# Optimization experiments

Measured on AMD Instinct MI355X. Metric: run time of the kernel, lower is better.

## Reference

```python
import jax, jax.numpy as jnp
import numpy as np

N = 8192      # nodes
E = 262144    # edges per graph (avg degree 32)
D_IN = 256
HID = 64
HEADS = 2
NEG_SLOPE = 0.2  # PyG GATConv leaky_relu slope


def _self_loops(ei, n):
    loop = jnp.arange(n, dtype=ei.dtype)
    return jnp.concatenate([ei[0], loop]), jnp.concatenate([ei[1], loop])


def gat_conv(x, src, dst, W, att_src, att_dst, b, concat):
    # PyG GATConv: h=[N,H,C]; alpha=softmax_dst(leaky_relu(a_s[src]+a_d[dst]))
    n = x.shape[0]
    H, C = att_src.shape
    h = (x @ W).reshape(n, H, C)
    a_s = (h * att_src).sum(-1)           # [N,H]
    a_d = (h * att_dst).sum(-1)           # [N,H]
    e = jax.nn.leaky_relu(a_s[src] + a_d[dst], NEG_SLOPE)  # [Etot,H]
    e = e - jax.ops.segment_max(e, dst, num_segments=n)[dst]
    e = jnp.exp(e)
    denom = jax.ops.segment_sum(e, dst, num_segments=n)[dst] + 1e-16
    alpha = e / denom                     # edge softmax per target node
    msg = h[src] * alpha[:, :, None]      # [Etot,H,C]
    out = jax.ops.segment_sum(msg, dst, num_segments=n)  # [N,H,C]
    out = out.reshape(n, H * C) if concat else out.mean(axis=1)
    return out + b


def gcn_conv(x, src, dst, W, b):
    # PyG GCNConv: D^{-1/2}(A+I)D^{-1/2} X W + b (self loops already appended)
    n = x.shape[0]
    h = x @ W
    deg = jax.ops.segment_sum(jnp.ones_like(src, jnp.float32), dst, num_segments=n)
    dinv = jax.lax.rsqrt(jnp.maximum(deg, 1.0))
    norm = dinv[src] * dinv[dst]          # [Etot]
    return jax.ops.segment_sum(h[src] * norm[:, None], dst, num_segments=n) + b


def cross_attn(q_in, kv_in, Wq, bq, Wk, bk, Wv, bv, Wo, bo, num_heads):
    n, d = q_in.shape
    hd = d // num_heads
    q = (q_in @ Wq + bq).reshape(n, num_heads, hd)
    k = (kv_in @ Wk + bk).reshape(n, num_heads, hd)
    v = (kv_in @ Wv + bv).reshape(n, num_heads, hd)
    scores = jnp.einsum('qhd,khd->hqk', q, k) / np.sqrt(hd).astype(np.float32)
    attn = jax.nn.softmax(scores, axis=-1)                 # [H,N,N]
    out = jnp.einsum('hqk,khd->qhd', attn, v).reshape(n, d) @ Wo + bo
    weights = attn.mean(axis=0)[None]                      # [1,N,N] avg heads (torch default)
    return out, weights


def setup_inputs():
    key = jax.random.key(0)
    ks = jax.random.split(key, 24)
    w = lambda k, s: jax.random.normal(k, s, jnp.float32) * 0.05
    inp = {
        'x': jax.random.normal(ks[0], (N, D_IN), jnp.float32),
        'edge_index_tkg': jax.random.randint(ks[1], (2, E), 0, N, jnp.int64 if jax.config.jax_enable_x64 else jnp.int32),
        'edge_index_ekg': jax.random.randint(ks[2], (2, E), 0, N, jnp.int64 if jax.config.jax_enable_x64 else jnp.int32),
        # GAT layer 1: heads=2, concat=True
        'gat1_W': w(ks[3], (D_IN, HEADS * HID)),
        'gat1_att_src': w(ks[4], (HEADS, HID)),
        'gat1_att_dst': w(ks[5], (HEADS, HID)),
        'gat1_b': jnp.zeros((HEADS * HID,), jnp.float32),
        # GAT layer 2: heads=1, concat=False
        'gat2_W': w(ks[6], (HEADS * HID, HID)),
        'gat2_att_src': w(ks[7], (1, HID)),
        'gat2_att_dst': w(ks[8], (1, HID)),
        'gat2_b': jnp.zeros((HID,), jnp.float32),
        # GCN layers
        'gcn1_W': w(ks[9], (D_IN, HID)),
        'gcn1_b': jnp.zeros((HID,), jnp.float32),
        'gcn2_W': w(ks[10], (HID, HID)),
        'gcn2_b': jnp.zeros((HID,), jnp.float32),
        # cross attention (hidden=64, 2 heads)
        'Wq': w(ks[11], (HID, HID)), 'bq': jnp.zeros((HID,), jnp.float32),
        'Wk': w(ks[12], (HID, HID)), 'bk': jnp.zeros((HID,), jnp.float32),
        'Wv': w(ks[13], (HID, HID)), 'bv': jnp.zeros((HID,), jnp.float32),
        'Wo': w(ks[14], (HID, HID)), 'bo': jnp.zeros((HID,), jnp.float32),
        # MLP head
        'fc1_W': w(ks[15], (2 * HID, HID)), 'fc1_b': jnp.zeros((HID,), jnp.float32),
        'fc2_W': w(ks[16], (HID, 1)), 'fc2_b': jnp.zeros((1,), jnp.float32),
    }
    return inp


def reference(x, edge_index_tkg, edge_index_ekg,
              gat1_W, gat1_att_src, gat1_att_dst, gat1_b,
              gat2_W, gat2_att_src, gat2_att_dst, gat2_b,
              gcn1_W, gcn1_b, gcn2_W, gcn2_b,
              Wq, bq, Wk, bk, Wv, bv, Wo, bo,
              fc1_W, fc1_b, fc2_W, fc2_b):
    n = x.shape[0]
    src_t, dst_t = _self_loops(edge_index_tkg, n)
    src_e, dst_e = _self_loops(edge_index_ekg, n)

    h_tkg = jax.nn.elu(gat_conv(x, src_t, dst_t, gat1_W, gat1_att_src, gat1_att_dst, gat1_b, True))
    h_tkg = jax.nn.elu(gat_conv(h_tkg, src_t, dst_t, gat2_W, gat2_att_src, gat2_att_dst, gat2_b, False))

    h_ekg = jax.nn.relu(gcn_conv(x, src_e, dst_e, gcn1_W, gcn1_b))
    h_ekg = jax.nn.relu(gcn_conv(h_ekg, src_e, dst_e, gcn2_W, gcn2_b))

    h_attn, attn_weights = cross_attn(h_tkg, h_ekg, Wq, bq, Wk, bk, Wv, bv, Wo, bo, HEADS)

    h_fused = jnp.concatenate([h_tkg, h_attn], axis=1)   # [N, 2*HID]
    pred = (jax.nn.relu(h_fused @ fc1_W + fc1_b) @ fc2_W + fc2_b).squeeze(-1)
    return pred, attn_weights
```

## Files before the change

kernel.cpp:

```cpp
#include <hip/hip_runtime.h>
#include <cstdint>
#include <cstddef>

#define NN 8192
#define EE 262144
#define ET 270336

using short8  = __attribute__((ext_vector_type(8))) short;
using floatx4 = __attribute__((ext_vector_type(4))) float;

__device__ __forceinline__ unsigned short f2bf(float f) {
  unsigned int u = __float_as_uint(f);
  u += 0x7fffu + ((u >> 16) & 1u);
  return (unsigned short)(u >> 16);
}

__global__ void edge_hist2_k(const int* __restrict__ ei_t, const int* __restrict__ ei_e,
                             int* __restrict__ cnt_t, int* __restrict__ cnt_e) {
  int idx = blockIdx.x * 256 + threadIdx.x;
  int g = idx >= ET;
  int e = g ? idx - ET : idx;
  const int* ei = g ? ei_e : ei_t;
  int* cnt = g ? cnt_e : cnt_t;
  int d = (e < EE) ? ei[EE + e] : (e - EE);
  atomicAdd(&cnt[d], 1);
}

__global__ void scan2_k(int* cnt_t, int* off_t, int* cnt_e, int* off_e) {
  int* cnt = blockIdx.x ? cnt_e : cnt_t;
  int* off = blockIdx.x ? off_e : off_t;
  __shared__ int s[1024];
  int t = threadIdx.x;
  int v[8]; int base = t * 8; int sum = 0;
  #pragma unroll
  for (int j = 0; j < 8; ++j) { v[j] = cnt[base + j]; sum += v[j]; }
  s[t] = sum; __syncthreads();
  for (int o = 1; o < 1024; o <<= 1) {
    int x = (t >= o) ? s[t - o] : 0;
    __syncthreads();
    s[t] += x;
    __syncthreads();
  }
  int excl = s[t] - sum;
  #pragma unroll
  for (int j = 0; j < 8; ++j) { off[base + j] = excl; cnt[base + j] = excl; excl += v[j]; }
  if (t == 1023) off[NN] = excl;
}

__global__ void edge_scatter2_k(const int* __restrict__ ei_t, const int* __restrict__ ei_e,
                                int* __restrict__ pos_t, int* __restrict__ pos_e,
                                int* __restrict__ srcs_t, int* __restrict__ srcs_e) {
  int idx = blockIdx.x * 256 + threadIdx.x;
  int g = idx >= ET;
  int e = g ? idx - ET : idx;
  const int* ei = g ? ei_e : ei_t;
  int* pos = g ? pos_e : pos_t;
  int* srcs = g ? srcs_e : srcs_t;
  int sv, d;
  if (e < EE) { sv = ei[e]; d = ei[EE + e]; } else { sv = d = e - EE; }
  int p = atomicAdd(&pos[d], 1);
  srcs[p] = sv;
}

__device__ __forceinline__ void gemm_core(const float* __restrict__ A, int lda, int K,
                                          const float* __restrict__ Bs, int row0, int col,
                                          float acc[8]) {
  #pragma unroll
  for (int r = 0; r < 8; ++r) acc[r] = 0.f;
  for (int k = 0; k < K; k += 4) {
    float b0 = Bs[(k + 0) * 32 + col], b1 = Bs[(k + 1) * 32 + col];
    float b2 = Bs[(k + 2) * 32 + col], b3 = Bs[(k + 3) * 32 + col];
    #pragma unroll
    for (int r = 0; r < 8; ++r) {
      const float4 a4 = *(const float4*)(A + (size_t)(row0 + r) * lda + k);
      acc[r] = fmaf(a4.x, b0, acc[r]);
      acc[r] = fmaf(a4.y, b1, acc[r]);
      acc[r] = fmaf(a4.z, b2, acc[r]);
      acc[r] = fmaf(a4.w, b3, acc[r]);
    }
  }
}

__global__ __launch_bounds__(256) void mm_x_k(const float* __restrict__ x,
    const float* __restrict__ Wgat, const float* __restrict__ Wgcn,
    const float* __restrict__ as_w, const float* __restrict__ ad_w,
    float* __restrict__ h1, float* __restrict__ hg1,
    float* __restrict__ a_s1, float* __restrict__ a_d1) {
  __shared__ float Bs[256 * 32];
  const int tid = threadIdx.x, by = blockIdx.y;
  const bool gat = by < 4;
  const int NC = gat ? 128 : 64;
  const int c0 = gat ? by * 32 : (by - 4) * 32;
  const float* B = gat ? Wgat : Wgcn;
  for (int idx = tid; idx < 256 * 32; idx += 256)
    Bs[idx] = B[(idx >> 5) * NC + c0 + (idx & 31)];
  __syncthreads();
  const int row0 = blockIdx.x * 64 + (tid >> 5) * 8;
  const int col = tid & 31;
  float acc[8];
  gemm_core(x, 256, 256, Bs, row0, col, acc);
  if (gat) {
    #pragma unroll
    for (int r = 0; r < 8; ++r) h1[(size_t)(row0 + r) * 128 + c0 + col] = acc[r];
    const int head = c0 >> 6;
    const float asw = as_w[head * 64 + (c0 & 63) + col];
    const float adw = ad_w[head * 64 + (c0 & 63) + col];
    float ps[8], pd[8];
    #pragma unroll
    for (int r = 0; r < 8; ++r) { ps[r] = acc[r] * asw; pd[r] = acc[r] * adw; }
    #pragma unroll
    for (int m = 16; m >= 1; m >>= 1)
      #pragma unroll
      for (int r = 0; r < 8; ++r) { ps[r] += __shfl_xor(ps[r], m); pd[r] += __shfl_xor(pd[r], m); }
    if (col == 0) {
      #pragma unroll
      for (int r = 0; r < 8; ++r) {
        atomicAdd(&a_s1[(row0 + r) * 2 + head], ps[r]);
        atomicAdd(&a_d1[(row0 + r) * 2 + head], pd[r]);
      }
    }
  } else {
    #pragma unroll
    for (int r = 0; r < 8; ++r) hg1[(size_t)(row0 + r) * 64 + c0 + col] = acc[r];
  }
}

template<int H, int C>
__device__ __forceinline__ void gat_agg_body(const float* __restrict__ h,
    const float* __restrict__ a_s, const float* __restrict__ a_d,
    const int* __restrict__ off, const int* __restrict__ srcs,
    const float* __restrict__ bias, float* __restrict__ out, int ldout, int b) {
  constexpr int HC = H * C;
  const int tid = threadIdx.x;
  const int hd = tid / C;
  const int r0 = off[b], r1 = off[b + 1];
  __shared__ int s_src[HC];
  __shared__ float s_w[HC][H];
  float ad[H];
  #pragma unroll
  for (int hh = 0; hh < H; ++hh) ad[hh] = a_d[b * H + hh];
  float acc = 0.f, den = 0.f;
  for (int base = r0; base < r1; base += HC) {
    __syncthreads();
    int e = base + tid;
    if (e < r1) {
      int sv = srcs[e];
      s_src[tid] = sv;
      #pragma unroll
      for (int hh = 0; hh < H; ++hh) {
        float xv = a_s[sv * H + hh] + ad[hh];
        xv = xv > 0.f ? xv : 0.2f * xv;
        s_w[tid][hh] = __expf(xv);
      }
    }
    __syncthreads();
    int cnt = min(HC, r1 - base);
    for (int j = 0; j < cnt; ++j) {
      float wv = s_w[j][hd];
      den += wv;
      acc = fmaf(wv, h[(size_t)s_src[j] * HC + tid], acc);
    }
  }
  float o = acc / den + bias[tid];
  out[(size_t)b * ldout + tid] = o > 0.f ? o : (__expf(o) - 1.f);
}

template<int H, int C>
__global__ void gat_agg_k(const float* __restrict__ h, const float* __restrict__ a_s,
                          const float* __restrict__ a_d, const int* __restrict__ off,
                          const int* __restrict__ srcs, const float* __restrict__ bias,
                          float* __restrict__ out, int ldout) {
  gat_agg_body<H, C>(h, a_s, a_d, off, srcs, bias, out, ldout, blockIdx.x);
}

__global__ __launch_bounds__(128) void agg1_k(
    const float* __restrict__ h1, const float* __restrict__ a_s1, const float* __restrict__ a_d1,
    const int* __restrict__ off_t, const int* __restrict__ src_t,
    const float* __restrict__ gat1_b, float* __restrict__ g1out,
    const float* __restrict__ hg1, const int* __restrict__ off_e, const int* __restrict__ src_e,
    const float* __restrict__ gcn1_b, const float* __restrict__ gcn2_W, float* __restrict__ h2g) {
  const int tid = threadIdx.x;
  if (blockIdx.x < NN) {
    gat_agg_body<2, 64>(h1, a_s1, a_d1, off_t, src_t, gat1_b, g1out, 128, blockIdx.x);
  } else {
    const int nb = (blockIdx.x - NN) * 2;
    const int sub = tid >> 6, t = tid & 63;
    const int node = nb + sub;
    __shared__ int s_src2[2][64];
    __shared__ float s_nrm2[2][64];
    __shared__ float s_row2[2][64];
    const int r0 = off_e[node], r1 = off_e[node + 1];
    const int cA = off_e[nb + 1] - off_e[nb];
    const int cB = off_e[nb + 2] - off_e[nb + 1];
    const int trips = (max(cA, cB) + 63) >> 6;
    float dinv_b = rsqrtf((float)max(r1 - r0, 1));
    float acc = 0.f;
    for (int it = 0; it < trips; ++it) {
      __syncthreads();
      int e = r0 + it * 64 + t;
      if (e < r1) {
        int sv = src_e[e];
        s_src2[sub][t] = sv;
        int ds = off_e[sv + 1] - off_e[sv];
        s_nrm2[sub][t] = dinv_b * rsqrtf((float)max(ds, 1));
      }
      __syncthreads();
      int cnt = min(64, r1 - (r0 + it * 64));
      for (int j = 0; j < cnt; ++j)
        acc = fmaf(s_nrm2[sub][j], hg1[(size_t)s_src2[sub][j] * 64 + t], acc);
    }
    s_row2[sub][t] = fmaxf(acc + gcn1_b[t], 0.f);
    __syncthreads();
    float acc2 = 0.f;
    for (int k = 0; k < 64; ++k)
      acc2 = fmaf(s_row2[sub][k], gcn2_W[k * 64 + t], acc2);
    h2g[(size_t)node * 64 + t] = acc2;
  }
}

__global__ __launch_bounds__(256) void mm2_k(
    const float* __restrict__ g1out, const float* __restrict__ gat2_W,
    const float* __restrict__ gat2_as, const float* __restrict__ gat2_ad,
    float* __restrict__ h2, float* __restrict__ a_s2, float* __restrict__ a_d2,
    const float* __restrict__ h2g, const int* __restrict__ off_e, const int* __restrict__ src_e,
    const float* __restrict__ gcn2_b, float* __restrict__ hekg) {
  const int tid = threadIdx.x;
  if (blockIdx.x < 256) {
    __shared__ float Bs[128 * 32];
    const int bx = blockIdx.x & 127;
    const int c0 = (blockIdx.x >> 7) * 32;
    for (int idx = tid; idx < 128 * 32; idx += 256)
      Bs[idx] = gat2_W[(idx >> 5) * 64 + c0 + (idx & 31)];
    __syncthreads();
    const int row0 = bx * 64 + (tid >> 5) * 8;
    const int col = tid & 31;
    float acc[8];
    gemm_core(g1out, 128, 128, Bs, row0, col, acc);
    const float asw = gat2_as[c0 + col];
    const float adw = gat2_ad[c0 + col];
    float ps[8], pd[8];
    #pragma unroll
    for (int r = 0; r < 8; ++r) {
      h2[(size_t)(row0 + r) * 64 + c0 + col] = acc[r];
      ps[r] = acc[r] * asw; pd[r] = acc[r] * adw;
    }
    #pragma unroll
    for (int m = 16; m >= 1; m >>= 1)
      #pragma unroll
      for (int r = 0; r < 8; ++r) { ps[r] += __shfl_xor(ps[r], m); pd[r] += __shfl_xor(pd[r], m); }
    if (col == 0) {
      #pragma unroll
      for (int r = 0; r < 8; ++r) {
        atomicAdd(&a_s2[row0 + r], ps[r]);
        atomicAdd(&a_d2[row0 + r], pd[r]);
      }
    }
  } else {
    const int nb = (blockIdx.x - 256) * 4;
    const int sub = tid >> 6, t = tid & 63;
    const int node = nb + sub;
    __shared__ int s_src4[4][64];
    __shared__ float s_nrm4[4][64];
    const int r0 = off_e[node], r1 = off_e[node + 1];
    int cmax = 0;
    #pragma unroll
    for (int i = 0; i < 4; ++i) cmax = max(cmax, off_e[nb + i + 1] - off_e[nb + i]);
    const int trips = (cmax + 63) >> 6;
    float dinv_b = rsqrtf((float)max(r1 - r0, 1));
    float acc = 0.f;
    for (int it = 0; it < trips; ++it) {
      __syncthreads();
      int e = r0 + it * 64 + t;
      if (e < r1) {
        int sv = src_e[e];
        s_src4[sub][t] = sv;
        int ds = off_e[sv + 1] - off_e[sv];
        s_nrm4[sub][t] = dinv_b * rsqrtf((float)max(ds, 1));
      }
      __syncthreads();
      int cnt = min(64, r1 - (r0 + it * 64));
      for (int j = 0; j < cnt; ++j)
        acc = fmaf(s_nrm4[sub][j], h2g[(size_t)s_src4[sub][j] * 64 + t], acc);
    }
    hekg[(size_t)node * 64 + t] = fmaxf(acc + gcn2_b[t], 0.f);
  }
}

__global__ __launch_bounds__(256) void mm_qkv_k(const float* __restrict__ htkg,
    const float* __restrict__ hekg,
    const float* __restrict__ Wq, const float* __restrict__ bq,
    const float* __restrict__ Wk, const float* __restrict__ bk,
    const float* __restrict__ Wv, const float* __restrict__ bv,
    unsigned short* __restrict__ qb, unsigned short* __restrict__ kb,
    unsigned short* __restrict__ Vt) {
  __shared__ float Bs[64 * 32];
  __shared__ float Ts[32][65];
  const int tid = threadIdx.x, by = blockIdx.y;
  const int kind = by >> 1;
  const int c0 = (by & 1) * 32;
  const float* A = (kind == 0) ? htkg : hekg;
  const float* B = (kind == 0) ? Wq : (kind == 1) ? Wk : Wv;
  const float* bias = (kind == 0) ? bq : (kind == 1) ? bk : bv;
  for (int idx = tid; idx < 64 * 32; idx += 256)
    Bs[idx] = B[(idx >> 5) * 64 + c0 + (idx & 31)];
  __syncthreads();
  const int row0 = blockIdx.x * 64 + (tid >> 5) * 8;
  const int col = tid & 31;
  float acc[8];
  gemm_core(A, 64, 64, Bs, row0, col, acc);
  const float bb = bias[c0 + col];
  if (kind == 0) {
    const float SCL = 0.17677669529663687f * 1.4426950408889634f;
    #pragma unroll
    for (int r = 0; r < 8; ++r)
      qb[(size_t)(row0 + r) * 64 + c0 + col] = f2bf((acc[r] + bb) * SCL);
  } else if (kind == 1) {
    #pragma unroll
    for (int r = 0; r < 8; ++r)
      kb[(size_t)(row0 + r) * 64 + c0 + col] = f2bf(acc[r] + bb);
  } else {
    const int rl = (tid >> 5) * 8;
    #pragma unroll
    for (int r = 0; r < 8; ++r) Ts[col][rl + r] = acc[r] + bb;
    __syncthreads();
    const int c = tid >> 3, rr = (tid & 7) * 8;
    short8 pk;
    #pragma unroll
    for (int j = 0; j < 8; ++j) pk[j] = (short)f2bf(Ts[c][rr + j]);
    *(short8*)(Vt + (size_t)(c0 + c) * NN + blockIdx.x * 64 + rr) = pk;
  }
}

__global__ __launch_bounds__(256, 4) void att_pass1(const unsigned short* __restrict__ qb,
                                                    const unsigned short* __restrict__ kb,
                                                    float* __restrict__ lrow) {
  const int tid = threadIdx.x;
  const int lane = tid & 63, wv = tid >> 6;
  const int ql = lane & 15, quad = lane >> 4;
  const int qt0 = (blockIdx.x >> 1) * 16;
  const int khalf = blockIdx.x & 1;
  const floatx4 zf = {0.f, 0.f, 0.f, 0.f};
  short8 qf[2];
  #pragma unroll
  for (int h = 0; h < 2; ++h)
    qf[h] = *(const short8*)(qb + (size_t)(qt0 + ql) * 64 + h * 32 + quad * 8);
  float lacc[2][4];
  #pragma unroll
  for (int h = 0; h < 2; ++h)
    #pragma unroll
    for (int r = 0; r < 4; ++r) lacc[h][r] = 0.f;
  int kbase = khalf * 4096 + wv * 1024;
  for (int it = 0; it < 32; ++it, kbase += 32) {
    short8 kf[2][2];
    #pragma unroll
    for (int kt = 0; kt < 2; ++kt)
      #pragma unroll
      for (int h = 0; h < 2; ++h)
        kf[kt][h] = *(const short8*)(kb + (size_t)(kbase + kt * 16 + ql) * 64 + h * 32 + quad * 8);
    #pragma unroll
    for (int h = 0; h < 2; ++h)
      #pragma unroll
      for (int kt = 0; kt < 2; ++kt) {
        floatx4 s = __builtin_amdgcn_mfma_f32_16x16x32_bf16(qf[h], kf[kt][h], zf, 0, 0, 0);
        #pragma unroll
        for (int r = 0; r < 4; ++r) lacc[h][r] += __builtin_amdgcn_exp2f(s[r]);
      }
  }
  #pragma unroll
  for (int o = 8; o >= 1; o >>= 1)
    #pragma unroll
    for (int h = 0; h < 2; ++h)
      #pragma unroll
      for (int r = 0; r < 4; ++r)
        lacc[h][r] += __shfl_xor(lacc[h][r], o, 16);
  if (ql == 0) {
    #pragma unroll
    for (int h = 0; h < 2; ++h)
      #pragma unroll
      for (int r = 0; r < 4; ++r)
        atomicAdd(&lrow[(size_t)(qt0 + quad * 4 + r) * 2 + h], lacc[h][r]);
  }
}

__global__ __launch_bounds__(256, 4) void att_pass2(
    const unsigned short* __restrict__ qb, const unsigned short* __restrict__ kb,
    const unsigned short* __restrict__ Vt, const float* __restrict__ lrow,
    float* __restrict__ attn, float* __restrict__ Opart) {
  __shared__ __align__(16) float Esh[4][2][16 * 36];
  __shared__ float Osh[16 * 64];
  const int tid = threadIdx.x;
  const int lane = tid & 63, wv = tid >> 6;
  const int ql = lane & 15, quad = lane >> 4;
  const int qt0 = (blockIdx.x >> 1) * 16;
  const int khalf = blockIdx.x & 1;
  float* O = Opart + (size_t)khalf * NN * 64;
  const floatx4 zf = {0.f, 0.f, 0.f, 0.f};

  for (int idx = tid; idx < 16 * 64; idx += 256) Osh[idx] = 0.f;
  __syncthreads();

  short8 qf[2];
  #pragma unroll
  for (int h = 0; h < 2; ++h)
    qf[h] = *(const short8*)(qb + (size_t)(qt0 + ql) * 64 + h * 32 + quad * 8);

  float invl[2][4];
  #pragma unroll
  for (int h = 0; h < 2; ++h)
    #pragma unroll
    for (int r = 0; r < 4; ++r)
      invl[h][r] = 1.0f / lrow[(size_t)(qt0 + quad * 4 + r) * 2 + h];

  floatx4 oacc[2][2];
  #pragma unroll
  for (int h = 0; h < 2; ++h)
    #pragma unroll
    for (int hf = 0; hf < 2; ++hf) oacc[h][hf] = zf;

  int kbase = khalf * 4096 + wv * 1024;
  for (int it = 0; it < 32; ++it, kbase += 32) {
    short8 kf[2][2], vf[2][2];
    #pragma unroll
    for (int kt = 0; kt < 2; ++kt)
      #pragma unroll
      for (int h = 0; h < 2; ++h)
        kf[kt][h] = *(const short8*)(kb + (size_t)(kbase + kt * 16 + ql) * 64 + h * 32 + quad * 8);
    #pragma unroll
    for (int h = 0; h < 2; ++h)
      #pragma unroll
      for (int hf = 0; hf < 2; ++hf)
        vf[h][hf] = *(const short8*)(Vt + (size_t)(h * 32 + hf * 16 + ql) * NN + kbase + quad * 8);

    floatx4 p[2][2];
    #pragma unroll
    for (int h = 0; h < 2; ++h)
      #pragma unroll
      for (int kt = 0; kt < 2; ++kt) {
        floatx4 s = __builtin_amdgcn_mfma_f32_16x16x32_bf16(qf[h], kf[kt][h], zf, 0, 0, 0);
        #pragma unroll
        for (int r = 0; r < 4; ++r)
          p[h][kt][r] = __builtin_amdgcn_exp2f(s[r]) * invl[h][r];
      }
    #pragma unroll
    for (int kt = 0; kt < 2; ++kt)
      #pragma unroll
      for (int r = 0; r < 4; ++r) {
        size_t row = (size_t)(qt0 + quad * 4 + r);
        __builtin_nontemporal_store(0.5f * (p[0][kt][r] + p[1][kt][r]),
                                    &attn[row * NN + kbase + kt * 16 + ql]);
      }
    #pragma unroll
    for (int h = 0; h < 2; ++h)
      #pragma unroll
      for (int kt = 0; kt < 2; ++kt)
        #pragma unroll
        for (int r = 0; r < 4; ++r)
          Esh[wv][h][(quad * 4 + r) * 36 + kt * 16 + ql] = p[h][kt][r];
    #pragma unroll
    for (int h = 0; h < 2; ++h) {
      const float* ep = &Esh[wv][h][ql * 36 + quad * 8];
      float4 x0 = *(const float4*)ep;
      float4 x1 = *(const float4*)(ep + 4);
      short8 ef;
      ef[0] = (short)f2bf(x0.x); ef[1] = (short)f2bf(x0.y);
      ef[2] = (short)f2bf(x0.z); ef[3] = (short)f2bf(x0.w);
      ef[4] = (short)f2bf(x1.x); ef[5] = (short)f2bf(x1.y);
      ef[6] = (short)f2bf(x1.z); ef[7] = (short)f2bf(x1.w);
      #pragma unroll
      for (int hf = 0; hf < 2; ++hf)
        oacc[h][hf] = __builtin_amdgcn_mfma_f32_16x16x32_bf16(ef, vf[h][hf], oacc[h][hf], 0, 0, 0);
    }
  }
  #pragma unroll
  for (int h = 0; h < 2; ++h)
    #pragma unroll
    for (int hf = 0; hf < 2; ++hf)
      #pragma unroll
      for (int r = 0; r < 4; ++r)
        atomicAdd(&Osh[(quad * 4 + r) * 64 + h * 32 + hf * 16 + ql], oacc[h][hf][r]);
  __syncthreads();
  for (int idx = tid; idx < 16 * 64; idx += 256)
    O[(size_t)qt0 * 64 + idx] = Osh[idx];
}

__global__ __launch_bounds__(256) void tail_k(const float* __restrict__ Opart,
    const float* __restrict__ htkg, const float* __restrict__ Wo, const float* __restrict__ bo,
    const float* __restrict__ fc1W, const float* __restrict__ fc1b,
    const float* __restrict__ fc2W, const float* __restrict__ fc2b,
    float* __restrict__ pred) {
  __shared__ float Ws[8192];
  __shared__ float T1[2048];
  __shared__ float T2[2048];
  const int tid = threadIdx.x;
  const int col = tid & 63, rg = tid >> 6;
  const int rowbase = blockIdx.x * 32;
  for (int i = tid; i < 2048; i += 256) {
    size_t idx = (size_t)rowbase * 64 + i;
    T1[i] = Opart[idx] + Opart[(size_t)NN * 64 + idx];
  }
  for (int i = tid; i < 4096; i += 256) Ws[i] = Wo[i];
  const float rbo = bo[col], rf1b = fc1b[col], rf2 = fc2W[col], rf2b = fc2b[0];
  __syncthreads();
  float ha[8];
  #pragma unroll
  for (int r = 0; r < 8; ++r) {
    const int row = rg * 8 + r;
    float acc = rbo;
    for (int k = 0; k < 64; ++k) acc = fmaf(T1[row * 64 + k], Ws[k * 64 + col], acc);
    ha[r] = acc;
  }
  __syncthreads();
  #pragma unroll
  for (int r = 0; r < 8; ++r) T2[(rg * 8 + r) * 64 + col] = ha[r];
  for (int i = tid; i < 2048; i += 256) T1[i] = htkg[(size_t)rowbase * 64 + i];
  for (int i = tid; i < 8192; i += 256) Ws[i] = fc1W[i];
  __syncthreads();
  #pragma unroll
  for (int r = 0; r < 8; ++r) {
    const int row = rg * 8 + r;
    float acc = rf1b;
    for (int k = 0; k < 64; ++k) acc = fmaf(T1[row * 64 + k], Ws[k * 64 + col], acc);
    for (int k = 0; k < 64; ++k) acc = fmaf(T2[row * 64 + k], Ws[(64 + k) * 64 + col], acc);
    float y = fmaxf(acc, 0.f);
    float v = y * rf2;
    #pragma unroll
    for (int m = 32; m >= 1; m >>= 1) v += __shfl_xor(v, m);
    if (col == 0) pred[rowbase + row] = v + rf2b;
  }
}

extern "C" void kernel_launch(void* const* d_in, const int* in_sizes, int n_in,
                              void* d_out, int out_size, void* d_ws, size_t ws_size,
                              hipStream_t stream) {
  (void)in_sizes; (void)n_in; (void)out_size; (void)ws_size;
  const float* x       = (const float*)d_in[0];
  const int*   ei_t    = (const int*)d_in[1];
  const int*   ei_e    = (const int*)d_in[2];
  const float* gat1_W  = (const float*)d_in[3];
  const float* gat1_as = (const float*)d_in[4];
  const float* gat1_ad = (const float*)d_in[5];
  const float* gat1_b  = (const float*)d_in[6];
  const float* gat2_W  = (const float*)d_in[7];
  const float* gat2_as = (const float*)d_in[8];
  const float* gat2_ad = (const float*)d_in[9];
  const float* gat2_b  = (const float*)d_in[10];
  const float* gcn1_W  = (const float*)d_in[11];
  const float* gcn1_b  = (const float*)d_in[12];
  const float* gcn2_W  = (const float*)d_in[13];
  const float* gcn2_b  = (const float*)d_in[14];
  const float* Wq = (const float*)d_in[15]; const float* bq = (const float*)d_in[16];
  const float* Wk = (const float*)d_in[17]; const float* bk = (const float*)d_in[18];
  const float* Wv = (const float*)d_in[19]; const float* bv = (const float*)d_in[20];
  const float* Wo = (const float*)d_in[21]; const float* bo = (const float*)d_in[22];
  const float* fc1_W = (const float*)d_in[23]; const float* fc1_b = (const float*)d_in[24];
  const float* fc2_W = (const float*)d_in[25]; const float* fc2_b = (const float*)d_in[26];

  float* out  = (float*)d_out;
  float* attn = out + NN;

  char* wsp = (char*)d_ws;
  size_t ofs = 0;
  auto take = [&](size_t bytes) -> char* {
    char* p = wsp + ofs;
    ofs = (ofs + bytes + 255) & ~(size_t)255;
    return p;
  };
  int*   pos_t = (int*)take(NN * 4);
  int*   pos_e = (int*)take(NN * 4);
  float* lbuf  = (float*)take((size_t)NN * 2 * 4);
  float* a_s1  = (float*)take((size_t)NN * 2 * 4);
  float* a_d1  = (float*)take((size_t)NN * 2 * 4);
  float* a_s2  = (float*)take((size_t)NN * 4);
  float* a_d2  = (float*)take((size_t)NN * 4);
  const size_t zero_span = ofs;
  int* off_t = (int*)take((NN + 1) * 4);
  int* off_e = (int*)take((NN + 1) * 4);
  int* src_t = (int*)take((size_t)ET * 4);
  int* src_e = (int*)take((size_t)ET * 4);
  float* h1    = (float*)take((size_t)NN * 128 * 4);
  float* g1out = (float*)take((size_t)NN * 128 * 4);
  float* h2    = (float*)take((size_t)NN * 64 * 4);
  float* htkg  = (float*)take((size_t)NN * 64 * 4);
  float* hg1   = (float*)take((size_t)NN * 64 * 4);
  float* h2g   = (float*)take((size_t)NN * 64 * 4);
  float* hekg  = (float*)take((size_t)NN * 64 * 4);
  unsigned short* qb = (unsigned short*)take((size_t)NN * 64 * 2);
  unsigned short* kb = (unsigned short*)take((size_t)NN * 64 * 2);
  unsigned short* Vt = (unsigned short*)take((size_t)64 * NN * 2);
  float* Opart = (float*)take((size_t)2 * NN * 64 * 4);

  hipMemsetAsync(wsp, 0, zero_span, stream);

  edge_hist2_k<<<2 * ET / 256, 256, 0, stream>>>(ei_t, ei_e, pos_t, pos_e);
  scan2_k<<<2, 1024, 0, stream>>>(pos_t, off_t, pos_e, off_e);
  edge_scatter2_k<<<2 * ET / 256, 256, 0, stream>>>(ei_t, ei_e, pos_t, pos_e, src_t, src_e);

  mm_x_k<<<dim3(128, 6), 256, 0, stream>>>(x, gat1_W, gcn1_W, gat1_as, gat1_ad,
                                           h1, hg1, a_s1, a_d1);
  agg1_k<<<NN + NN / 2, 128, 0, stream>>>(h1, a_s1, a_d1, off_t, src_t, gat1_b, g1out,
                                          hg1, off_e, src_e, gcn1_b, gcn2_W, h2g);
  mm2_k<<<256 + NN / 4, 256, 0, stream>>>(g1out, gat2_W, gat2_as, gat2_ad, h2, a_s2, a_d2,
                                          h2g, off_e, src_e, gcn2_b, hekg);
  gat_agg_k<1, 64><<<NN, 64, 0, stream>>>(h2, a_s2, a_d2, off_t, src_t, gat2_b, htkg, 64);

  mm_qkv_k<<<dim3(128, 6), 256, 0, stream>>>(htkg, hekg, Wq, bq, Wk, bk, Wv, bv, qb, kb, Vt);

  att_pass1<<<1024, 256, 0, stream>>>(qb, kb, lbuf);
  att_pass2<<<1024, 256, 0, stream>>>(qb, kb, Vt, lbuf, attn, Opart);

  tail_k<<<256, 256, 0, stream>>>(Opart, htkg, Wo, bo, fc1_W, fc1_b, fc2_W, fc2_b, out);
}
```

Measured before the change: 668.8 us.

## Fuse attention row-sum and output passes into one kernel per query tile

Merges the two attention kernels into one. Each block now owns a full 16-row query tile and all 8192 keys, so the row sums are reduced in shared memory instead of through global atomics, and the partial-output buffer and its reduction in the tail kernel are removed. The attention-weight store now goes through shared memory so each lane writes float4 rows instead of scattered scalar nontemporal stores. The trade-off is half as many blocks (512) with longer per-block loops and no min-occupancy hint, which may reduce latency hiding.

```diff
diff --git a/kernel.cpp b/kernel.cpp
--- a/kernel.cpp
+++ b/kernel.cpp
@@ -331,26 +331,33 @@
   }
 }
 
-__global__ __launch_bounds__(256, 4) void att_pass1(const unsigned short* __restrict__ qb,
-                                                    const unsigned short* __restrict__ kb,
-                                                    float* __restrict__ lrow) {
+__global__ __launch_bounds__(256) void att_fused(
+    const unsigned short* __restrict__ qb, const unsigned short* __restrict__ kb,
+    const unsigned short* __restrict__ Vt,
+    float* __restrict__ attn, float* __restrict__ O) {
+  __shared__ __align__(16) float Esh[4][2][16 * 36];
+  __shared__ float lsh[4][16][2];
+  __shared__ float Osh[16 * 64];
   const int tid = threadIdx.x;
   const int lane = tid & 63, wv = tid >> 6;
   const int ql = lane & 15, quad = lane >> 4;
-  const int qt0 = (blockIdx.x >> 1) * 16;
-  const int khalf = blockIdx.x & 1;
+  const int qt0 = blockIdx.x * 16;
   const floatx4 zf = {0.f, 0.f, 0.f, 0.f};
+
+  for (int idx = tid; idx < 16 * 64; idx += 256) Osh[idx] = 0.f;
+
   short8 qf[2];
   #pragma unroll
   for (int h = 0; h < 2; ++h)
     qf[h] = *(const short8*)(qb + (size_t)(qt0 + ql) * 64 + h * 32 + quad * 8);
+
   float lacc[2][4];
   #pragma unroll
   for (int h = 0; h < 2; ++h)
     #pragma unroll
     for (int r = 0; r < 4; ++r) lacc[h][r] = 0.f;
-  int kbase = khalf * 4096 + wv * 1024;
-  for (int it = 0; it < 32; ++it, kbase += 32) {
+  int kbase = wv * 2048;
+  for (int it = 0; it < 64; ++it, kbase += 32) {
     short8 kf[2][2];
     #pragma unroll
     for (int kt = 0; kt < 2; ++kt)
@@ -378,47 +385,28 @@
     for (int h = 0; h < 2; ++h)
       #pragma unroll
       for (int r = 0; r < 4; ++r)
-        atomicAdd(&lrow[(size_t)(qt0 + quad * 4 + r) * 2 + h], lacc[h][r]);
-  }
-}
-
-__global__ __launch_bounds__(256, 4) void att_pass2(
-    const unsigned short* __restrict__ qb, const unsigned short* __restrict__ kb,
-    const unsigned short* __restrict__ Vt, const float* __restrict__ lrow,
-    float* __restrict__ attn, float* __restrict__ Opart) {
-  __shared__ __align__(16) float Esh[4][2][16 * 36];
-  __shared__ float Osh[16 * 64];
-  const int tid = threadIdx.x;
-  const int lane = tid & 63, wv = tid >> 6;
-  const int ql = lane & 15, quad = lane >> 4;
-  const int qt0 = (blockIdx.x >> 1) * 16;
-  const int khalf = blockIdx.x & 1;
-  float* O = Opart + (size_t)khalf * NN * 64;
-  const floatx4 zf = {0.f, 0.f, 0.f, 0.f};
-
-  for (int idx = tid; idx < 16 * 64; idx += 256) Osh[idx] = 0.f;
+        lsh[wv][quad * 4 + r][h] = lacc[h][r];
+  }
   __syncthreads();
-
-  short8 qf[2];
+  float invl[2][4];
   #pragma unroll
   for (int h = 0; h < 2; ++h)
-    qf[h] = *(const short8*)(qb + (size_t)(qt0 + ql) * 64 + h * 32 + quad * 8);
-
-  float invl[2][4];
+    #pragma unroll
+    for (int r = 0; r < 4; ++r) {
+      int row = quad * 4 + r;
+      invl[h][r] = 1.0f / (lsh[0][row][h] + lsh[1][row][h] + lsh[2][row][h] + lsh[3][row][h]);
+    }
+
+  floatx4 oacc[2][2];
   #pragma unroll
   for (int h = 0; h < 2; ++h)
     #pragma unroll
-    for (int r = 0; r < 4; ++r)
-      invl[h][r] = 1.0f / lrow[(size_t)(qt0 + quad * 4 + r) * 2 + h];
-
-  floatx4 oacc[2][2];
-  #pragma unroll
-  for (int h = 0; h < 2; ++h)
-    #pragma unroll
     for (int hf = 0; hf < 2; ++hf) oacc[h][hf] = zf;
 
-  int kbase = khalf * 4096 + wv * 1024;
-  for (int it = 0; it < 32; ++it, kbase += 32) {
+  const int r8 = lane >> 3;
+  const int c4 = (lane & 7) * 4;
+  kbase = wv * 2048;
+  for (int it = 0; it < 64; ++it, kbase += 32) {
     short8 kf[2][2], vf[2][2];
     #pragma unroll
     for (int kt = 0; kt < 2; ++kt)
@@ -442,20 +430,25 @@
           p[h][kt][r] = __builtin_amdgcn_exp2f(s[r]) * invl[h][r];
       }
     #pragma unroll
-    for (int kt = 0; kt < 2; ++kt)
-      #pragma unroll
-      for (int r = 0; r < 4; ++r) {
-        size_t row = (size_t)(qt0 + quad * 4 + r);
-        __builtin_nontemporal_store(0.5f * (p[0][kt][r] + p[1][kt][r]),
-                                    &attn[row * NN + kbase + kt * 16 + ql]);
-      }
-    #pragma unroll
     for (int h = 0; h < 2; ++h)
       #pragma unroll
       for (int kt = 0; kt < 2; ++kt)
         #pragma unroll
         for (int r = 0; r < 4; ++r)
           Esh[wv][h][(quad * 4 + r) * 36 + kt * 16 + ql] = p[h][kt][r];
+    {
+      const float4 a0 = *(const float4*)&Esh[wv][0][r8 * 36 + c4];
+      const float4 b0 = *(const float4*)&Esh[wv][1][r8 * 36 + c4];
+      const float4 a1 = *(const float4*)&Esh[wv][0][(r8 + 8) * 36 + c4];
+      const float4 b1 = *(const float4*)&Esh[wv][1][(r8 + 8) * 36 + c4];
+      float4 m0, m1;
+      m0.x = 0.5f * (a0.x + b0.x); m0.y = 0.5f * (a0.y + b0.y);
+      m0.z = 0.5f * (a0.z + b0.z); m0.w = 0.5f * (a0.w + b0.w);
+      m1.x = 0.5f * (a1.x + b1.x); m1.y = 0.5f * (a1.y + b1.y);
+      m1.z = 0.5f * (a1.z + b1.z); m1.w = 0.5f * (a1.w + b1.w);
+      *(float4*)&attn[(size_t)(qt0 + r8) * NN + kbase + c4] = m0;
+      *(float4*)&attn[(size_t)(qt0 + r8 + 8) * NN + kbase + c4] = m1;
+    }
     #pragma unroll
     for (int h = 0; h < 2; ++h) {
       const float* ep = &Esh[wv][h][ql * 36 + quad * 8];
@@ -483,7 +476,7 @@
     O[(size_t)qt0 * 64 + idx] = Osh[idx];
 }
 
-__global__ __launch_bounds__(256) void tail_k(const float* __restrict__ Opart,
+__global__ __launch_bounds__(256) void tail_k(const float* __restrict__ O,
     const float* __restrict__ htkg, const float* __restrict__ Wo, const float* __restrict__ bo,
     const float* __restrict__ fc1W, const float* __restrict__ fc1b,
     const float* __restrict__ fc2W, const float* __restrict__ fc2b,
@@ -494,10 +487,7 @@
   const int tid = threadIdx.x;
   const int col = tid & 63, rg = tid >> 6;
   const int rowbase = blockIdx.x * 32;
-  for (int i = tid; i < 2048; i += 256) {
-    size_t idx = (size_t)rowbase * 64 + i;
-    T1[i] = Opart[idx] + Opart[(size_t)NN * 64 + idx];
-  }
+  for (int i = tid; i < 2048; i += 256) T1[i] = O[(size_t)rowbase * 64 + i];
   for (int i = tid; i < 4096; i += 256) Ws[i] = Wo[i];
   const float rbo = bo[col], rf1b = fc1b[col], rf2 = fc2W[col], rf2b = fc2b[0];
   __syncthreads();
@@ -567,7 +557,6 @@
   };
   int*   pos_t = (int*)take(NN * 4);
   int*   pos_e = (int*)take(NN * 4);
-  float* lbuf  = (float*)take((size_t)NN * 2 * 4);
   float* a_s1  = (float*)take((size_t)NN * 2 * 4);
   float* a_d1  = (float*)take((size_t)NN * 2 * 4);
   float* a_s2  = (float*)take((size_t)NN * 4);
@@ -587,7 +576,7 @@
   unsigned short* qb = (unsigned short*)take((size_t)NN * 64 * 2);
   unsigned short* kb = (unsigned short*)take((size_t)NN * 64 * 2);
   unsigned short* Vt = (unsigned short*)take((size_t)64 * NN * 2);
-  float* Opart = (float*)take((size_t)2 * NN * 64 * 4);
+  float* Obuf  = (float*)take((size_t)NN * 64 * 4);
 
   hipMemsetAsync(wsp, 0, zero_span, stream);
 
@@ -605,8 +594,7 @@
 
   mm_qkv_k<<<dim3(128, 6), 256, 0, stream>>>(htkg, hekg, Wq, bq, Wk, bk, Wv, bv, qb, kb, Vt);
 
-  att_pass1<<<1024, 256, 0, stream>>>(qb, kb, lbuf);
-  att_pass2<<<1024, 256, 0, stream>>>(qb, kb, Vt, lbuf, attn, Opart);
-
-  tail_k<<<256, 256, 0, stream>>>(Opart, htkg, Wo, bo, fc1_W, fc1_b, fc2_W, fc2_b, out);
-}
+  att_fused<<<512, 256, 0, stream>>>(qb, kb, Vt, attn, Obuf);
+
+  tail_k<<<256, 256, 0, stream>>>(Obuf, htkg, Wo, bo, fc1_W, fc1_b, fc2_W, fc2_b, out);
+}
```

Result: no change. 662.1 us (-1.0%).
